# Performance work log

Hardware: AMD Instinct MI355X
Metric: run time of the kernel (lower is better)

Reference implementation:

```python
import math
import jax, jax.numpy as jnp
import numpy as np

N_HEAD = 16

def _rope_sin_cos(pos, head_dim, base=10000.0):
    # matches build_sin_cos(seq_len, dim=head_dim//2): inv = base^(-2i/head_dim)
    inv = jnp.exp(jnp.arange(0, head_dim, 2, dtype=jnp.float32) * (-math.log(base) / head_dim))  # (Dh//2,)
    ang = pos[:, None].astype(jnp.float32) * inv[None, :]  # (T, Dh//2)
    return jnp.sin(ang), jnp.cos(ang)

def _apply_rope(q, k, sin, cos):
    # q, k: (B, T, H, Dh); sin/cos: (T, Dh//2)
    half = q.shape[-1] // 2
    s = sin[None, :, None, :]
    c = cos[None, :, None, :]
    q1, q2 = q[..., :half], q[..., half:]
    k1, k2 = k[..., :half], k[..., half:]
    q_rot = jnp.concatenate([q1 * c - q2 * s, q2 * c + q1 * s], axis=-1)
    k_rot = jnp.concatenate([k1 * c - k2 * s, k2 * c + k1 * s], axis=-1)
    return q_rot, k_rot

def setup_inputs() -> dict:
    key = jax.random.key(0)
    k0, k1, k2 = jax.random.split(key, 3)
    B, T, D = 2, 2048, 2048
    x = jax.random.normal(k0, (B, T, D), dtype=jnp.float32)
    w_qkv = jax.random.normal(k1, (3 * D, D), dtype=jnp.float32) * (D ** -0.5)
    w_proj = jax.random.normal(k2, (D, D), dtype=jnp.float32) * (D ** -0.5)
    return {"x": x, "w_qkv": w_qkv, "w_proj": w_proj, "seq_offset": 0}

def reference(x, w_qkv, w_proj, seq_offset):
    # Single-device (world_size=1) ring attention: one hop, so the online
    # lse-merge is the identity; exact causal flash attention + RoPE.
    B, T, D = x.shape
    H = N_HEAD
    Dh = D // H
    qkv = (x @ w_qkv.T).reshape(B, T, 3, H, Dh)
    q, k, v = qkv[:, :, 0], qkv[:, :, 1], qkv[:, :, 2]  # (B, T, H, Dh)
    pos = seq_offset + jnp.arange(T)
    sin, cos = _rope_sin_cos(pos, Dh)
    q, k = _apply_rope(q, k, sin, cos)
    scale = 1.0 / math.sqrt(Dh)  # flash-attn default softmax_scale
    scores = jnp.einsum('bthd,bshd->bhts', q, k) * scale  # (B, H, T, T)
    causal = jnp.tril(jnp.ones((T, T), dtype=bool))
    scores = jnp.where(causal[None, None], scores, -jnp.inf)
    attn = jax.nn.softmax(scores, axis=-1)
    ctx = jnp.einsum('bhts,bshd->bthd', attn, v)  # (B, T, H, Dh)
    out = ctx.reshape(B, T, D) @ w_proj.T
    return out
```

## Files before the change

### kernel.cpp

```cpp
#include <hip/hip_runtime.h>
#include <math.h>

typedef __bf16 bf16x8 __attribute__((ext_vector_type(8)));
typedef float f32x4 __attribute__((ext_vector_type(4)));
typedef unsigned short u16;
typedef unsigned short u16x4 __attribute__((ext_vector_type(4)));
typedef unsigned short u16x8 __attribute__((ext_vector_type(8)));
typedef unsigned int u32;

#define AS1 __attribute__((address_space(1)))
#define AS3 __attribute__((address_space(3)))

static __device__ __forceinline__ float bf2f(u16 u) {
  union { u32 i; float f; } v; v.i = ((u32)u) << 16; return v.f;
}
static __device__ __forceinline__ u16 f2bf(float f) {
  union { __bf16 b; u16 u; } v; v.b = (__bf16)f; return v.u;
}

__global__ __launch_bounds__(256)
void conv_all(const float* __restrict__ x, const float* __restrict__ wq,
              const float* __restrict__ wp, u16* __restrict__ dst) {
  const int gid = blockIdx.x * 256 + threadIdx.x;
  const float* src;
  int off;
  if (gid < 2097152) { src = x; off = gid; }
  else if (gid < 2097152 + 3145728) { src = wq; off = gid - 2097152; }
  else { src = wp; off = gid - (2097152 + 3145728); }
  const float4 v = ((const float4*)src)[off];
  u16x4 p = {f2bf(v.x), f2bf(v.y), f2bf(v.z), f2bf(v.w)};
  ((u16x4*)dst)[gid] = p;
}

template <bool CF32>
__global__ __launch_bounds__(256, 4)
void gemm_bt(const u16* __restrict__ A, const u16* __restrict__ B,
             void* __restrict__ Cp, int M, int N, int K) {
  __shared__ __align__(16) u16 As[128 * 64];
  __shared__ __align__(16) u16 Bs[128 * 64];
  const int tid = threadIdx.x;
  const int lane = tid & 63;
  const int wid = tid >> 6;
  const int wr = wid >> 1, wc = wid & 1;
  const int l15 = lane & 15, l4 = lane >> 4;
  const int m0 = blockIdx.y * 128, n0 = blockIdx.x * 128;

  int grow[4], gkc[4];
#pragma unroll
  for (int i = 0; i < 4; ++i) {
    const int idx = i * 256 + tid;
    grow[i] = idx >> 3;
    gkc[i] = ((idx & 7) ^ (grow[i] & 7)) * 8;
  }

  const f32x4 fzero = {0.f, 0.f, 0.f, 0.f};
  f32x4 acc[4][4];
#pragma unroll
  for (int i = 0; i < 4; ++i)
#pragma unroll
    for (int j = 0; j < 4; ++j) acc[i][j] = fzero;

  for (int kt = 0; kt < K; kt += 64) {
#pragma unroll
    for (int i = 0; i < 4; ++i) {
      __builtin_amdgcn_global_load_lds(
          (AS1 void*)(A + (size_t)(m0 + grow[i]) * K + kt + gkc[i]),
          (AS3 void*)(As + (size_t)(i * 256 + tid) * 8), 16, 0, 0);
      __builtin_amdgcn_global_load_lds(
          (AS1 void*)(B + (size_t)(n0 + grow[i]) * K + kt + gkc[i]),
          (AS3 void*)(Bs + (size_t)(i * 256 + tid) * 8), 16, 0, 0);
    }
    __syncthreads();
    bf16x8 af[4][2], bfr[4][2];
#pragma unroll
    for (int m = 0; m < 4; ++m) {
      const int ra = wr * 64 + m * 16 + l15;
#pragma unroll
      for (int ks = 0; ks < 2; ++ks)
        af[m][ks] = *(const bf16x8*)&As[ra * 64 + (((ks * 4 + l4) ^ (ra & 7)) << 3)];
    }
#pragma unroll
    for (int n = 0; n < 4; ++n) {
      const int rb = wc * 64 + n * 16 + l15;
#pragma unroll
      for (int ks = 0; ks < 2; ++ks)
        bfr[n][ks] = *(const bf16x8*)&Bs[rb * 64 + (((ks * 4 + l4) ^ (rb & 7)) << 3)];
    }
#pragma unroll
    for (int m = 0; m < 4; ++m)
#pragma unroll
      for (int n = 0; n < 4; ++n) {
        acc[m][n] = __builtin_amdgcn_mfma_f32_16x16x32_bf16(af[m][0], bfr[n][0], acc[m][n], 0, 0, 0);
        acc[m][n] = __builtin_amdgcn_mfma_f32_16x16x32_bf16(af[m][1], bfr[n][1], acc[m][n], 0, 0, 0);
      }
    __syncthreads();
  }

#pragma unroll
  for (int m = 0; m < 4; ++m)
#pragma unroll
    for (int r = 0; r < 4; ++r) {
      const int gm = m0 + wr * 64 + m * 16 + l4 * 4 + r;
      if constexpr (CF32) {
        float* crow = (float*)Cp + (size_t)gm * N + n0 + wc * 64 + l15;
#pragma unroll
        for (int n = 0; n < 4; ++n) crow[n * 16] = acc[m][n][r];
      } else {
        u16* crow = (u16*)Cp + (size_t)gm * N + n0 + wc * 64 + l15;
#pragma unroll
        for (int n = 0; n < 4; ++n) crow[n * 16] = f2bf(acc[m][n][r]);
      }
    }
}

__global__ __launch_bounds__(256)
void rope_kernel(u16* __restrict__ qkv, const int* __restrict__ seq_off) {
  const int idx = blockIdx.x * 256 + threadIdx.x;
  const int d8 = idx & 7;
  const int h = (idx >> 3) & 15;
  const int t = (idx >> 7) & 2047;
  const int b = idx >> 18;
  const int d0 = d8 * 8;
  const float pos = (float)(seq_off[0] + t);
  const size_t base = ((size_t)(b * 2048 + t)) * 6144 + h * 128 + d0;
  const u16x8 qlo = *(const u16x8*)(qkv + base);
  const u16x8 qhi = *(const u16x8*)(qkv + base + 64);
  const u16x8 klo = *(const u16x8*)(qkv + base + 2048);
  const u16x8 khi = *(const u16x8*)(qkv + base + 2048 + 64);
  u16x8 qlo_o, qhi_o, klo_o, khi_o;
#pragma unroll
  for (int j = 0; j < 8; ++j) {
    const float inv = expf((float)(d0 + j) * (-0.14391156509731588f));
    float sv, cv;
    sincosf(pos * inv, &sv, &cv);
    const float q1 = bf2f(qlo[j]), q2 = bf2f(qhi[j]);
    qlo_o[j] = f2bf(q1 * cv - q2 * sv);
    qhi_o[j] = f2bf(q2 * cv + q1 * sv);
    const float k1 = bf2f(klo[j]), k2 = bf2f(khi[j]);
    klo_o[j] = f2bf(k1 * cv - k2 * sv);
    khi_o[j] = f2bf(k2 * cv + k1 * sv);
  }
  *(u16x8*)(qkv + base) = qlo_o;
  *(u16x8*)(qkv + base + 64) = qhi_o;
  *(u16x8*)(qkv + base + 2048) = klo_o;
  *(u16x8*)(qkv + base + 2048 + 64) = khi_o;
}

__global__ __launch_bounds__(256, 2)
void attn_kernel(const u16* __restrict__ qkv, u16* __restrict__ ctx) {
  __shared__ __align__(16) u16 kbuf[2][2][32 * 128];
  __shared__ __align__(16) u16 vbuf[2][2][128 * 32];
  __shared__ __align__(16) u16 Plds[4][2][16 * 32];
  const int tid = threadIdx.x, lane = tid & 63, w = tid >> 6;
  const int l15 = lane & 15, l4 = lane >> 4;
  const int lin = blockIdx.y * gridDim.x + blockIdx.x;
  const int xcd = lin & 7;
  const int iw = lin >> 3;
  const int bh = xcd + 8 * (iw & 3);
  const int qp = iw >> 2;
  const int b = bh >> 4, h = bh & 15;
  const u16* Qb = qkv + (size_t)b * 2048 * 6144 + h * 128;
  const u16* Kb = Qb + 2048;
  const u16* Vb = Qb + 4096;

  const int sp = tid & 15;
  const int sB = tid >> 4;
  const int sgp = sB & 1;
  const int swg = (((sp >> 2) ^ (sB & 3)) << 3) + ((sp & 3) << 1);
  const int ks0 = (w * 2 + 0) * 64 + lane;
  const int ks1 = (w * 2 + 1) * 64 + lane;
  const int kr0 = ks0 >> 4, kc0 = (ks0 & 15) ^ (kr0 & 15);
  const int kr1 = ks1 >> 4, kc1 = (ks1 & 15) ^ (kr1 & 15);

  const float scale = 0.08838834764831845f;
  const float M0 = 12.0f;
  const f32x4 fzero = {0.f, 0.f, 0.f, 0.f};

  for (int pass = 0; pass < 2; ++pass) {
    const int qt = pass ? qp : (31 - qp);
    const int q0 = qt * 64 + w * 16;
    const int nt64 = qt + 1;

    bf16x8 qf[4];
#pragma unroll
    for (int c = 0; c < 4; ++c)
      qf[c] = *(const bf16x8*)(Qb + (size_t)(q0 + l15) * 6144 + c * 32 + l4 * 8);

    f32x4 o[8];
#pragma unroll
    for (int ch = 0; ch < 8; ++ch) o[ch] = fzero;
    float lpart[4] = {0.f, 0.f, 0.f, 0.f};

    __syncthreads();
#pragma unroll
    for (int hh = 0; hh < 2; ++hh) {
      __builtin_amdgcn_global_load_lds(
          (AS1 void*)(Kb + (size_t)(hh * 32 + kr0) * 6144 + kc0 * 8),
          (AS3 void*)(&kbuf[0][hh][(w * 2 + 0) * 512]), 16, 0, 0);
      __builtin_amdgcn_global_load_lds(
          (AS1 void*)(Kb + (size_t)(hh * 32 + kr1) * 6144 + kc1 * 8),
          (AS3 void*)(&kbuf[0][hh][(w * 2 + 1) * 512]), 16, 0, 0);
      const u16* vp = Vb + (size_t)(hh * 32 + 2 * sp) * 6144 + 8 * sB;
      const u16x8 v0 = *(const u16x8*)vp;
      const u16x8 v1 = *(const u16x8*)(vp + 6144);
#pragma unroll
      for (int e = 0; e < 8; ++e) {
        const int s = e ^ sgp;
        const int dh = 8 * sB + s;
        *(u32*)&vbuf[0][hh][dh * 32 + swg] = (u32)v0[s] | ((u32)v1[s] << 16);
      }
    }
    __syncthreads();

    for (int t = 0; t < nt64; ++t) {
      const int cur = t & 1, nxtb = cur ^ 1;
      const int kv0 = t * 64;
      const bool has_next = (t + 1 < nt64);
      u16x8 va0, va1, vb0, vb1;
      if (has_next) {
        const u16* vp = Vb + (size_t)(kv0 + 64 + 2 * sp) * 6144 + 8 * sB;
        va0 = *(const u16x8*)vp;
        va1 = *(const u16x8*)(vp + 6144);
        const u16* vp2 = vp + (size_t)32 * 6144;
        vb0 = *(const u16x8*)vp2;
        vb1 = *(const u16x8*)(vp2 + 6144);
      }
      f32x4 sv[4];
      sv[0] = fzero; sv[1] = fzero; sv[2] = fzero; sv[3] = fzero;
#pragma unroll
      for (int hh = 0; hh < 2; ++hh) {
#pragma unroll
        for (int c = 0; c < 4; ++c) {
          const bf16x8 kf = *(const bf16x8*)&kbuf[cur][hh][l15 * 128 + (((c * 4 + l4) ^ l15) << 3)];
          sv[hh * 2] = __builtin_amdgcn_mfma_f32_16x16x32_bf16(qf[c], kf, sv[hh * 2], 0, 0, 0);
        }
#pragma unroll
        for (int c = 0; c < 4; ++c) {
          const bf16x8 kf = *(const bf16x8*)&kbuf[cur][hh][(16 + l15) * 128 + (((c * 4 + l4) ^ l15) << 3)];
          sv[hh * 2 + 1] = __builtin_amdgcn_mfma_f32_16x16x32_bf16(qf[c], kf, sv[hh * 2 + 1], 0, 0, 0);
        }
      }
      if (has_next) {
#pragma unroll
        for (int hh = 0; hh < 2; ++hh) {
          __builtin_amdgcn_global_load_lds(
              (AS1 void*)(Kb + (size_t)(kv0 + 64 + hh * 32 + kr0) * 6144 + kc0 * 8),
              (AS3 void*)(&kbuf[nxtb][hh][(w * 2 + 0) * 512]), 16, 0, 0);
          __builtin_amdgcn_global_load_lds(
              (AS1 void*)(Kb + (size_t)(kv0 + 64 + hh * 32 + kr1) * 6144 + kc1 * 8),
              (AS3 void*)(&kbuf[nxtb][hh][(w * 2 + 1) * 512]), 16, 0, 0);
        }
      }
#pragma unroll
      for (int hh = 0; hh < 2; ++hh) {
        const int kb0 = kv0 + hh * 32;
        if (kb0 + 31 <= q0) {
#pragma unroll
          for (int r = 0; r < 4; ++r) {
            const float p0 = __expf(fmaf(sv[hh * 2][r], scale, -M0));
            const float p1 = __expf(fmaf(sv[hh * 2 + 1][r], scale, -M0));
            lpart[r] += p0 + p1;
            const int row = l4 * 4 + r;
            const int g0 = ((l15 >> 3) ^ l4) & 3;
            const int g1 = (((l15 >> 3) | 2) ^ l4) & 3;
            Plds[w][hh][row * 32 + g0 * 8 + (l15 & 7)] = f2bf(p0);
            Plds[w][hh][row * 32 + g1 * 8 + (l15 & 7)] = f2bf(p1);
          }
        } else {
#pragma unroll
          for (int r = 0; r < 4; ++r) {
            const int qg = q0 + l4 * 4 + r;
            const float p0 = (kb0 + l15 <= qg) ? __expf(fmaf(sv[hh * 2][r], scale, -M0)) : 0.f;
            const float p1 = (kb0 + 16 + l15 <= qg) ? __expf(fmaf(sv[hh * 2 + 1][r], scale, -M0)) : 0.f;
            lpart[r] += p0 + p1;
            const int row = l4 * 4 + r;
            const int g0 = ((l15 >> 3) ^ l4) & 3;
            const int g1 = (((l15 >> 3) | 2) ^ l4) & 3;
            Plds[w][hh][row * 32 + g0 * 8 + (l15 & 7)] = f2bf(p0);
            Plds[w][hh][row * 32 + g1 * 8 + (l15 & 7)] = f2bf(p1);
          }
        }
      }
      __syncthreads();
      const bf16x8 pa0 = *(const bf16x8*)&Plds[w][0][l15 * 32 + ((l4 ^ (l15 >> 2)) << 3)];
      const bf16x8 pa1 = *(const bf16x8*)&Plds[w][1][l15 * 32 + ((l4 ^ (l15 >> 2)) << 3)];
#pragma unroll
      for (int ch = 0; ch < 8; ++ch) {
        const int dh = ch * 16 + l15;
        const int g = (l4 ^ ((2 * ch + (l15 >> 3)) & 3)) << 3;
        const bf16x8 vf0 = *(const bf16x8*)&vbuf[cur][0][dh * 32 + g];
        o[ch] = __builtin_amdgcn_mfma_f32_16x16x32_bf16(pa0, vf0, o[ch], 0, 0, 0);
        const bf16x8 vf1 = *(const bf16x8*)&vbuf[cur][1][dh * 32 + g];
        o[ch] = __builtin_amdgcn_mfma_f32_16x16x32_bf16(pa1, vf1, o[ch], 0, 0, 0);
      }
      if (has_next) {
#pragma unroll
        for (int e = 0; e < 8; ++e) {
          const int s = e ^ sgp;
          const int dh = 8 * sB + s;
          *(u32*)&vbuf[nxtb][0][dh * 32 + swg] = (u32)va0[s] | ((u32)va1[s] << 16);
          *(u32*)&vbuf[nxtb][1][dh * 32 + swg] = (u32)vb0[s] | ((u32)vb1[s] << 16);
        }
      }
    }
    float invl[4];
#pragma unroll
    for (int r = 0; r < 4; ++r) {
      float l = lpart[r];
      l += __shfl_xor(l, 1);
      l += __shfl_xor(l, 2);
      l += __shfl_xor(l, 4);
      l += __shfl_xor(l, 8);
      invl[r] = 1.0f / l;
    }
#pragma unroll
    for (int ch = 0; ch < 8; ++ch)
#pragma unroll
      for (int r = 0; r < 4; ++r) {
        const int gq = q0 + l4 * 4 + r;
        ctx[(size_t)(b * 2048 + gq) * 2048 + h * 128 + ch * 16 + l15] =
            f2bf(o[ch][r] * invl[r]);
      }
  }
}

extern "C" void kernel_launch(void* const* d_in, const int* in_sizes, int n_in,
                              void* d_out, int out_size, void* d_ws, size_t ws_size,
                              hipStream_t stream) {
  const float* x     = (const float*)d_in[0];
  const float* wqkv  = (const float*)d_in[1];
  const float* wproj = (const float*)d_in[2];
  const int*   soff  = (const int*)d_in[3];
  float* out = (float*)d_out;

  u16* wsu    = (u16*)d_ws;
  u16* xb     = wsu;
  u16* wqkvb  = xb + 8388608;
  u16* wprojb = wqkvb + 12582912;
  u16* qkv    = wprojb + 4194304;
  u16* ctx    = xb;

  conv_all<<<24576, 256, 0, stream>>>(x, wqkv, wproj, wsu);

  gemm_bt<false><<<dim3(48, 32), 256, 0, stream>>>(xb, wqkvb, qkv, 4096, 6144, 2048);
  rope_kernel<<<2048, 256, 0, stream>>>(qkv, soff);
  attn_kernel<<<dim3(16, 32), 256, 0, stream>>>(qkv, ctx);
  gemm_bt<true><<<dim3(16, 32), 256, 0, stream>>>(ctx, wprojb, out, 4096, 2048, 2048);
}
```

Measured before the change: 259.9 us.

## Enlarge attention query tile to 128 rows with two row groups per wave

Each block now handles a 128-row query tile, with each wave owning 32 rows as two 16-row MFMA groups. This replaces the two-pass pairing of a short and a long 64-row tile. Every K/V tile loaded into LDS is reused across twice as many query rows, halving K/V traffic and barriers per unit of work. In exchange it raises register pressure (doubled accumulators and Q fragments), and blocks become unbalanced because the causal work per block now varies, whereas the old pairing was balanced.

```diff
diff --git a/kernel.cpp b/kernel.cpp
--- a/kernel.cpp
+++ b/kernel.cpp
@@ -150,14 +150,14 @@
 void attn_kernel(const u16* __restrict__ qkv, u16* __restrict__ ctx) {
   __shared__ __align__(16) u16 kbuf[2][2][32 * 128];
   __shared__ __align__(16) u16 vbuf[2][2][128 * 32];
-  __shared__ __align__(16) u16 Plds[4][2][16 * 32];
+  __shared__ __align__(16) u16 Plds[4][2][2][16 * 32];
   const int tid = threadIdx.x, lane = tid & 63, w = tid >> 6;
   const int l15 = lane & 15, l4 = lane >> 4;
-  const int lin = blockIdx.y * gridDim.x + blockIdx.x;
+  const int lin = blockIdx.x;
   const int xcd = lin & 7;
   const int iw = lin >> 3;
   const int bh = xcd + 8 * (iw & 3);
-  const int qp = iw >> 2;
+  const int qt = 15 - (iw >> 2);
   const int b = bh >> 4, h = bh & 15;
   const u16* Qb = qkv + (size_t)b * 2048 * 6144 + h * 128;
   const u16* Kb = Qb + 2048;
@@ -176,137 +176,153 @@
   const float M0 = 12.0f;
   const f32x4 fzero = {0.f, 0.f, 0.f, 0.f};
 
-  for (int pass = 0; pass < 2; ++pass) {
-    const int qt = pass ? qp : (31 - qp);
-    const int q0 = qt * 64 + w * 16;
-    const int nt64 = qt + 1;
-
-    bf16x8 qf[4];
+  const int q0w = qt * 128 + w * 32;
+  const int nt64 = qt * 2 + 2;
+
+  bf16x8 qf[2][4];
+#pragma unroll
+  for (int rg = 0; rg < 2; ++rg)
 #pragma unroll
     for (int c = 0; c < 4; ++c)
-      qf[c] = *(const bf16x8*)(Qb + (size_t)(q0 + l15) * 6144 + c * 32 + l4 * 8);
-
-    f32x4 o[8];
-#pragma unroll
-    for (int ch = 0; ch < 8; ++ch) o[ch] = fzero;
-    float lpart[4] = {0.f, 0.f, 0.f, 0.f};
-
+      qf[rg][c] = *(const bf16x8*)(Qb + (size_t)(q0w + rg * 16 + l15) * 6144 + c * 32 + l4 * 8);
+
+  f32x4 o[2][8];
+#pragma unroll
+  for (int rg = 0; rg < 2; ++rg)
+#pragma unroll
+    for (int ch = 0; ch < 8; ++ch) o[rg][ch] = fzero;
+  float lpart[2][4] = {{0.f, 0.f, 0.f, 0.f}, {0.f, 0.f, 0.f, 0.f}};
+
+#pragma unroll
+  for (int hh = 0; hh < 2; ++hh) {
+    __builtin_amdgcn_global_load_lds(
+        (AS1 void*)(Kb + (size_t)(hh * 32 + kr0) * 6144 + kc0 * 8),
+        (AS3 void*)(&kbuf[0][hh][(w * 2 + 0) * 512]), 16, 0, 0);
+    __builtin_amdgcn_global_load_lds(
+        (AS1 void*)(Kb + (size_t)(hh * 32 + kr1) * 6144 + kc1 * 8),
+        (AS3 void*)(&kbuf[0][hh][(w * 2 + 1) * 512]), 16, 0, 0);
+    const u16* vp = Vb + (size_t)(hh * 32 + 2 * sp) * 6144 + 8 * sB;
+    const u16x8 v0 = *(const u16x8*)vp;
+    const u16x8 v1 = *(const u16x8*)(vp + 6144);
+#pragma unroll
+    for (int e = 0; e < 8; ++e) {
+      const int s = e ^ sgp;
+      const int dh = 8 * sB + s;
+      *(u32*)&vbuf[0][hh][dh * 32 + swg] = (u32)v0[s] | ((u32)v1[s] << 16);
+    }
+  }
+  __syncthreads();
+
+  for (int t = 0; t < nt64; ++t) {
+    const int cur = t & 1, nxtb = cur ^ 1;
+    const int kv0 = t * 64;
+    const bool has_next = (t + 1 < nt64);
+    u16x8 va0, va1, vb0, vb1;
+    if (has_next) {
+      const u16* vp = Vb + (size_t)(kv0 + 64 + 2 * sp) * 6144 + 8 * sB;
+      va0 = *(const u16x8*)vp;
+      va1 = *(const u16x8*)(vp + 6144);
+      const u16* vp2 = vp + (size_t)32 * 6144;
+      vb0 = *(const u16x8*)vp2;
+      vb1 = *(const u16x8*)(vp2 + 6144);
+    }
+    f32x4 sv[2][4];
+#pragma unroll
+    for (int rg = 0; rg < 2; ++rg)
+#pragma unroll
+      for (int i = 0; i < 4; ++i) sv[rg][i] = fzero;
+#pragma unroll
+    for (int hh = 0; hh < 2; ++hh) {
+#pragma unroll
+      for (int c = 0; c < 4; ++c) {
+        const bf16x8 kf = *(const bf16x8*)&kbuf[cur][hh][l15 * 128 + (((c * 4 + l4) ^ l15) << 3)];
+        sv[0][hh * 2] = __builtin_amdgcn_mfma_f32_16x16x32_bf16(qf[0][c], kf, sv[0][hh * 2], 0, 0, 0);
+        sv[1][hh * 2] = __builtin_amdgcn_mfma_f32_16x16x32_bf16(qf[1][c], kf, sv[1][hh * 2], 0, 0, 0);
+      }
+#pragma unroll
+      for (int c = 0; c < 4; ++c) {
+        const bf16x8 kf = *(const bf16x8*)&kbuf[cur][hh][(16 + l15) * 128 + (((c * 4 + l4) ^ l15) << 3)];
+        sv[0][hh * 2 + 1] = __builtin_amdgcn_mfma_f32_16x16x32_bf16(qf[0][c], kf, sv[0][hh * 2 + 1], 0, 0, 0);
+        sv[1][hh * 2 + 1] = __builtin_amdgcn_mfma_f32_16x16x32_bf16(qf[1][c], kf, sv[1][hh * 2 + 1], 0, 0, 0);
+      }
+    }
+    if (has_next) {
+#pragma unroll
+      for (int hh = 0; hh < 2; ++hh) {
+        __builtin_amdgcn_global_load_lds(
+            (AS1 void*)(Kb + (size_t)(kv0 + 64 + hh * 32 + kr0) * 6144 + kc0 * 8),
+            (AS3 void*)(&kbuf[nxtb][hh][(w * 2 + 0) * 512]), 16, 0, 0);
+        __builtin_amdgcn_global_load_lds(
+            (AS1 void*)(Kb + (size_t)(kv0 + 64 + hh * 32 + kr1) * 6144 + kc1 * 8),
+            (AS3 void*)(&kbuf[nxtb][hh][(w * 2 + 1) * 512]), 16, 0, 0);
+      }
+    }
+#pragma unroll
+    for (int rg = 0; rg < 2; ++rg) {
+      const int q0r = q0w + rg * 16;
+#pragma unroll
+      for (int hh = 0; hh < 2; ++hh) {
+        const int kb0 = kv0 + hh * 32;
+        if (kb0 + 31 <= q0r) {
+#pragma unroll
+          for (int r = 0; r < 4; ++r) {
+            const float p0 = __expf(fmaf(sv[rg][hh * 2][r], scale, -M0));
+            const float p1 = __expf(fmaf(sv[rg][hh * 2 + 1][r], scale, -M0));
+            lpart[rg][r] += p0 + p1;
+            const int row = l4 * 4 + r;
+            const int g0 = ((l15 >> 3) ^ l4) & 3;
+            const int g1 = (((l15 >> 3) | 2) ^ l4) & 3;
+            Plds[w][rg][hh][row * 32 + g0 * 8 + (l15 & 7)] = f2bf(p0);
+            Plds[w][rg][hh][row * 32 + g1 * 8 + (l15 & 7)] = f2bf(p1);
+          }
+        } else {
+#pragma unroll
+          for (int r = 0; r < 4; ++r) {
+            const int qg = q0r + l4 * 4 + r;
+            const float p0 = (kb0 + l15 <= qg) ? __expf(fmaf(sv[rg][hh * 2][r], scale, -M0)) : 0.f;
+            const float p1 = (kb0 + 16 + l15 <= qg) ? __expf(fmaf(sv[rg][hh * 2 + 1][r], scale, -M0)) : 0.f;
+            lpart[rg][r] += p0 + p1;
+            const int row = l4 * 4 + r;
+            const int g0 = ((l15 >> 3) ^ l4) & 3;
+            const int g1 = (((l15 >> 3) | 2) ^ l4) & 3;
+            Plds[w][rg][hh][row * 32 + g0 * 8 + (l15 & 7)] = f2bf(p0);
+            Plds[w][rg][hh][row * 32 + g1 * 8 + (l15 & 7)] = f2bf(p1);
+          }
+        }
+      }
+    }
     __syncthreads();
-#pragma unroll
-    for (int hh = 0; hh < 2; ++hh) {
-      __builtin_amdgcn_global_load_lds(
-          (AS1 void*)(Kb + (size_t)(hh * 32 + kr0) * 6144 + kc0 * 8),
-          (AS3 void*)(&kbuf[0][hh][(w * 2 + 0) * 512]), 16, 0, 0);
-      __builtin_amdgcn_global_load_lds(
-          (AS1 void*)(Kb + (size_t)(hh * 32 + kr1) * 6144 + kc1 * 8),
-          (AS3 void*)(&kbuf[0][hh][(w * 2 + 1) * 512]), 16, 0, 0);
-      const u16* vp = Vb + (size_t)(hh * 32 + 2 * sp) * 6144 + 8 * sB;
-      const u16x8 v0 = *(const u16x8*)vp;
-      const u16x8 v1 = *(const u16x8*)(vp + 6144);
+    const bf16x8 pa00 = *(const bf16x8*)&Plds[w][0][0][l15 * 32 + ((l4 ^ (l15 >> 2)) << 3)];
+    const bf16x8 pa01 = *(const bf16x8*)&Plds[w][0][1][l15 * 32 + ((l4 ^ (l15 >> 2)) << 3)];
+    const bf16x8 pa10 = *(const bf16x8*)&Plds[w][1][0][l15 * 32 + ((l4 ^ (l15 >> 2)) << 3)];
+    const bf16x8 pa11 = *(const bf16x8*)&Plds[w][1][1][l15 * 32 + ((l4 ^ (l15 >> 2)) << 3)];
+#pragma unroll
+    for (int ch = 0; ch < 8; ++ch) {
+      const int dh = ch * 16 + l15;
+      const int g = (l4 ^ ((2 * ch + (l15 >> 3)) & 3)) << 3;
+      const bf16x8 vf0 = *(const bf16x8*)&vbuf[cur][0][dh * 32 + g];
+      o[0][ch] = __builtin_amdgcn_mfma_f32_16x16x32_bf16(pa00, vf0, o[0][ch], 0, 0, 0);
+      o[1][ch] = __builtin_amdgcn_mfma_f32_16x16x32_bf16(pa10, vf0, o[1][ch], 0, 0, 0);
+      const bf16x8 vf1 = *(const bf16x8*)&vbuf[cur][1][dh * 32 + g];
+      o[0][ch] = __builtin_amdgcn_mfma_f32_16x16x32_bf16(pa01, vf1, o[0][ch], 0, 0, 0);
+      o[1][ch] = __builtin_amdgcn_mfma_f32_16x16x32_bf16(pa11, vf1, o[1][ch], 0, 0, 0);
+    }
+    if (has_next) {
 #pragma unroll
       for (int e = 0; e < 8; ++e) {
         const int s = e ^ sgp;
         const int dh = 8 * sB + s;
-        *(u32*)&vbuf[0][hh][dh * 32 + swg] = (u32)v0[s] | ((u32)v1[s] << 16);
-      }
-    }
-    __syncthreads();
-
-    for (int t = 0; t < nt64; ++t) {
-      const int cur = t & 1, nxtb = cur ^ 1;
-      const int kv0 = t * 64;
-      const bool has_next = (t + 1 < nt64);
-      u16x8 va0, va1, vb0, vb1;
-      if (has_next) {
-        const u16* vp = Vb + (size_t)(kv0 + 64 + 2 * sp) * 6144 + 8 * sB;
-        va0 = *(const u16x8*)vp;
-        va1 = *(const u16x8*)(vp + 6144);
-        const u16* vp2 = vp + (size_t)32 * 6144;
-        vb0 = *(const u16x8*)vp2;
-        vb1 = *(const u16x8*)(vp2 + 6144);
-      }
-      f32x4 sv[4];
-      sv[0] = fzero; sv[1] = fzero; sv[2] = fzero; sv[3] = fzero;
-#pragma unroll
-      for (int hh = 0; hh < 2; ++hh) {
-#pragma unroll
-        for (int c = 0; c < 4; ++c) {
-          const bf16x8 kf = *(const bf16x8*)&kbuf[cur][hh][l15 * 128 + (((c * 4 + l4) ^ l15) << 3)];
-          sv[hh * 2] = __builtin_amdgcn_mfma_f32_16x16x32_bf16(qf[c], kf, sv[hh * 2], 0, 0, 0);
-        }
-#pragma unroll
-        for (int c = 0; c < 4; ++c) {
-          const bf16x8 kf = *(const bf16x8*)&kbuf[cur][hh][(16 + l15) * 128 + (((c * 4 + l4) ^ l15) << 3)];
-          sv[hh * 2 + 1] = __builtin_amdgcn_mfma_f32_16x16x32_bf16(qf[c], kf, sv[hh * 2 + 1], 0, 0, 0);
-        }
-      }
-      if (has_next) {
-#pragma unroll
-        for (int hh = 0; hh < 2; ++hh) {
-          __builtin_amdgcn_global_load_lds(
-              (AS1 void*)(Kb + (size_t)(kv0 + 64 + hh * 32 + kr0) * 6144 + kc0 * 8),
-              (AS3 void*)(&kbuf[nxtb][hh][(w * 2 + 0) * 512]), 16, 0, 0);
-          __builtin_amdgcn_global_load_lds(
-              (AS1 void*)(Kb + (size_t)(kv0 + 64 + hh * 32 + kr1) * 6144 + kc1 * 8),
-              (AS3 void*)(&kbuf[nxtb][hh][(w * 2 + 1) * 512]), 16, 0, 0);
-        }
-      }
-#pragma unroll
-      for (int hh = 0; hh < 2; ++hh) {
-        const int kb0 = kv0 + hh * 32;
-        if (kb0 + 31 <= q0) {
-#pragma unroll
-          for (int r = 0; r < 4; ++r) {
-            const float p0 = __expf(fmaf(sv[hh * 2][r], scale, -M0));
-            const float p1 = __expf(fmaf(sv[hh * 2 + 1][r], scale, -M0));
-            lpart[r] += p0 + p1;
-            const int row = l4 * 4 + r;
-            const int g0 = ((l15 >> 3) ^ l4) & 3;
-            const int g1 = (((l15 >> 3) | 2) ^ l4) & 3;
-            Plds[w][hh][row * 32 + g0 * 8 + (l15 & 7)] = f2bf(p0);
-            Plds[w][hh][row * 32 + g1 * 8 + (l15 & 7)] = f2bf(p1);
-          }
-        } else {
-#pragma unroll
-          for (int r = 0; r < 4; ++r) {
-            const int qg = q0 + l4 * 4 + r;
-            const float p0 = (kb0 + l15 <= qg) ? __expf(fmaf(sv[hh * 2][r], scale, -M0)) : 0.f;
-            const float p1 = (kb0 + 16 + l15 <= qg) ? __expf(fmaf(sv[hh * 2 + 1][r], scale, -M0)) : 0.f;
-            lpart[r] += p0 + p1;
-            const int row = l4 * 4 + r;
-            const int g0 = ((l15 >> 3) ^ l4) & 3;
-            const int g1 = (((l15 >> 3) | 2) ^ l4) & 3;
-            Plds[w][hh][row * 32 + g0 * 8 + (l15 & 7)] = f2bf(p0);
-            Plds[w][hh][row * 32 + g1 * 8 + (l15 & 7)] = f2bf(p1);
-          }
-        }
-      }
-      __syncthreads();
-      const bf16x8 pa0 = *(const bf16x8*)&Plds[w][0][l15 * 32 + ((l4 ^ (l15 >> 2)) << 3)];
-      const bf16x8 pa1 = *(const bf16x8*)&Plds[w][1][l15 * 32 + ((l4 ^ (l15 >> 2)) << 3)];
-#pragma unroll
-      for (int ch = 0; ch < 8; ++ch) {
-        const int dh = ch * 16 + l15;
-        const int g = (l4 ^ ((2 * ch + (l15 >> 3)) & 3)) << 3;
-        const bf16x8 vf0 = *(const bf16x8*)&vbuf[cur][0][dh * 32 + g];
-        o[ch] = __builtin_amdgcn_mfma_f32_16x16x32_bf16(pa0, vf0, o[ch], 0, 0, 0);
-        const bf16x8 vf1 = *(const bf16x8*)&vbuf[cur][1][dh * 32 + g];
-        o[ch] = __builtin_amdgcn_mfma_f32_16x16x32_bf16(pa1, vf1, o[ch], 0, 0, 0);
-      }
-      if (has_next) {
-#pragma unroll
-        for (int e = 0; e < 8; ++e) {
-          const int s = e ^ sgp;
-          const int dh = 8 * sB + s;
-          *(u32*)&vbuf[nxtb][0][dh * 32 + swg] = (u32)va0[s] | ((u32)va1[s] << 16);
-          *(u32*)&vbuf[nxtb][1][dh * 32 + swg] = (u32)vb0[s] | ((u32)vb1[s] << 16);
-        }
-      }
-    }
+        *(u32*)&vbuf[nxtb][0][dh * 32 + swg] = (u32)va0[s] | ((u32)va1[s] << 16);
+        *(u32*)&vbuf[nxtb][1][dh * 32 + swg] = (u32)vb0[s] | ((u32)vb1[s] << 16);
+      }
+    }
+  }
+#pragma unroll
+  for (int rg = 0; rg < 2; ++rg) {
     float invl[4];
 #pragma unroll
     for (int r = 0; r < 4; ++r) {
-      float l = lpart[r];
+      float l = lpart[rg][r];
       l += __shfl_xor(l, 1);
       l += __shfl_xor(l, 2);
       l += __shfl_xor(l, 4);
@@ -317,9 +333,9 @@
     for (int ch = 0; ch < 8; ++ch)
 #pragma unroll
       for (int r = 0; r < 4; ++r) {
-        const int gq = q0 + l4 * 4 + r;
+        const int gq = q0w + rg * 16 + l4 * 4 + r;
         ctx[(size_t)(b * 2048 + gq) * 2048 + h * 128 + ch * 16 + l15] =
-            f2bf(o[ch][r] * invl[r]);
+            f2bf(o[rg][ch][r] * invl[r]);
       }
   }
 }
@@ -344,6 +360,6 @@
 
   gemm_bt<false><<<dim3(48, 32), 256, 0, stream>>>(xb, wqkvb, qkv, 4096, 6144, 2048);
   rope_kernel<<<2048, 256, 0, stream>>>(qkv, soff);
-  attn_kernel<<<dim3(16, 32), 256, 0, stream>>>(qkv, ctx);
+  attn_kernel<<<512, 256, 0, stream>>>(qkv, ctx);
   gemm_bt<true><<<dim3(16, 32), 256, 0, stream>>>(ctx, wprojb, out, 4096, 2048, 2048);
 }
```

Measured after the change: 253.0 us. 2.7% less time.
